# Kernel tuning notes

Hardware: AMD Instinct MI355X
Metric: run time of the kernel (lower is better)

Reference implementation:

```python
import jax, jax.numpy as jnp
import numpy as np

N_NODES = 100000
N_EDGES = 800000
F_IN, HID, N_CLS = 256, 128, 32


def setup_inputs() -> dict:
    key = jax.random.key(0)
    k1, k2, k3, k4, k5 = jax.random.split(key, 5)
    features = jax.random.normal(k1, (N_NODES, F_IN), dtype=jnp.float32)
    # random directed edges with no self loops (so add_remaining_self_loops == append all loops)
    src = jax.random.randint(k2, (N_EDGES,), 0, N_NODES)
    off = jax.random.randint(k3, (N_EDGES,), 1, N_NODES)
    dst = (src + off) % N_NODES
    edge_index = jnp.stack([src, dst]).astype(jnp.int64)
    # Glorot-style params for the two GCNConv layers
    W1 = jax.random.normal(k4, (F_IN, HID), dtype=jnp.float32) * (1.0 / np.sqrt(F_IN))
    b1 = jnp.zeros((HID,), dtype=jnp.float32)
    W2 = jax.random.normal(k5, (HID, N_CLS), dtype=jnp.float32) * (1.0 / np.sqrt(HID))
    b2 = jnp.zeros((N_CLS,), dtype=jnp.float32)
    return {"features": features, "edge_index": edge_index, "W1": W1, "b1": b1, "W2": W2, "b2": b2}


def _gcn_conv(x, W, b, src, dst, norm, n):
    xw = x @ W                                  # [N, d_out] dense GEMM
    msg = xw[src] * norm[:, None]               # gather + scale, [E, d_out]
    out = jax.ops.segment_sum(msg, dst, num_segments=n)  # scatter-add to targets
    return out + b


def reference(features, edge_index, W1, b1, W2, b2):
    n = features.shape[0]
    # add_remaining_self_loops (input has none, so append all)
    loops = jnp.arange(n, dtype=edge_index.dtype)
    src = jnp.concatenate([edge_index[0], loops])
    dst = jnp.concatenate([edge_index[1], loops])
    # gcn_norm: deg over targets, sym normalization deg^-1/2 A deg^-1/2
    deg = jax.ops.segment_sum(jnp.ones_like(src, dtype=features.dtype), dst, num_segments=n)
    dinv = jnp.where(deg > 0, jax.lax.rsqrt(deg), 0.0)
    norm = dinv[src] * dinv[dst]
    x = _gcn_conv(features, W1, b1, src, dst, norm, n)
    x = jax.nn.relu(x)
    # dropout is identity at inference (training=False)
    x = _gcn_conv(x, W2, b2, src, dst, norm, n)
    return jax.nn.log_softmax(x, axis=1)
```

## Files before the change

### kernel.cpp

```cpp
#include <hip/hip_runtime.h>
#include <hip/hip_bf16.h>

typedef __bf16 bf16_t;
typedef __attribute__((ext_vector_type(8))) __bf16 bf16x8;
typedef __attribute__((ext_vector_type(4))) float f32x4;

__device__ inline void packB_one(const float* __restrict__ B, bf16_t* __restrict__ Bp,
                                 int N, int idx) {
    int j    = idx & 7;
    int lane = (idx >> 3) & 63;
    int st   = idx >> 9;
    int nt   = N >> 4;
    int s = st / nt, t = st - s * nt;
    int k = s * 32 + (lane >> 4) * 8 + j;
    int n = t * 16 + (lane & 15);
    Bp[idx] = (bf16_t)B[(size_t)k * N + n];
}

__global__ __launch_bounds__(256) void k_front(
        const float* __restrict__ W1, bf16_t* __restrict__ Bp1,
        const float* __restrict__ W2, bf16_t* __restrict__ Bp2,
        const int* __restrict__ dst, int* __restrict__ deg, int E) {
    int b = blockIdx.x, t = threadIdx.x;
    const int PACK_BLOCKS = (32768 + 4096) / 256;
    if (b < PACK_BLOCKS) {
        int idx = b * 256 + t;
        if (idx < 32768) packB_one(W1, Bp1, 128, idx);
        else             packB_one(W2, Bp2, 32, idx - 32768);
        return;
    }
    int i = (b - PACK_BLOCKS) * 1024 + t * 4;
    if (i + 4 <= E) {
        int4 v = *(const int4*)(dst + i);
        atomicAdd(&deg[v.x], 1); atomicAdd(&deg[v.y], 1);
        atomicAdd(&deg[v.z], 1); atomicAdd(&deg[v.w], 1);
    } else {
#pragma unroll
        for (int j = 0; j < 4; ++j)
            if (i + j < E) atomicAdd(&deg[dst[i + j]], 1);
    }
}

__global__ __launch_bounds__(256) void k_dinv_scan1(const int* __restrict__ deg,
                                                    float* __restrict__ dinv,
                                                    int* __restrict__ bsum, int n) {
    __shared__ int red[256];
    int b = blockIdx.x, t = threadIdx.x;
    int base = b * 1024 + t * 4;
    int s = 0;
#pragma unroll
    for (int j = 0; j < 4; ++j) {
        int i = base + j;
        if (i < n) { int d = deg[i]; s += d; dinv[i] = rsqrtf((float)(d + 1)); }
    }
    red[t] = s;
    __syncthreads();
    for (int d = 128; d > 0; d >>= 1) {
        if (t < d) red[t] += red[t + d];
        __syncthreads();
    }
    if (t == 0) bsum[b] = red[0];
}

__global__ __launch_bounds__(256) void k_scan2(int* __restrict__ bsum, int nb,
                                               int* __restrict__ rowPtr, int n) {
    __shared__ int s[256];
    int t = threadIdx.x;
    int v = (t < nb) ? bsum[t] : 0;
    s[t] = v;
    __syncthreads();
    for (int d = 1; d < 256; d <<= 1) {
        int u = (t >= d) ? s[t - d] : 0;
        __syncthreads();
        s[t] += u;
        __syncthreads();
    }
    if (t < nb) bsum[t] = s[t] - v;
    if (t == 255) rowPtr[n] = s[255];
}

__global__ __launch_bounds__(256) void k_scan3(const int* __restrict__ deg,
                                               const int* __restrict__ bsum,
                                               int* __restrict__ rowPtr,
                                               int* __restrict__ cursor, int n) {
    __shared__ int red[256];
    int b = blockIdx.x, t = threadIdx.x;
    int base = b * 1024 + t * 4;
    int v[4]; int s = 0;
#pragma unroll
    for (int j = 0; j < 4; ++j) { int i = base + j; v[j] = (i < n) ? deg[i] : 0; s += v[j]; }
    red[t] = s;
    __syncthreads();
    for (int d = 1; d < 256; d <<= 1) {
        int u = (t >= d) ? red[t - d] : 0;
        __syncthreads();
        red[t] += u;
        __syncthreads();
    }
    int run = bsum[b] + red[t] - s;
#pragma unroll
    for (int j = 0; j < 4; ++j) {
        int i = base + j;
        if (i < n) { rowPtr[i] = run; cursor[i] = run; run += v[j]; }
    }
}

template <int KSTEPS, int NTILES>
__global__ __launch_bounds__(256) void k_gemm_scatter(
        const float* __restrict__ A, const bf16_t* __restrict__ Bp,
        bf16_t* __restrict__ C, int M, int gemmBlocks,
        const int* __restrict__ src, const int* __restrict__ dst,
        const float* __restrict__ dinv, int* __restrict__ cursor,
        int2* __restrict__ edata, int E) {
    int b = blockIdx.x, t = threadIdx.x;
    if (b < gemmBlocks) {
        int wave = (b * 256 + t) >> 6;
        if (wave * 16 >= M) return;
        int lane = t & 63;
        int r16 = lane & 15, quad = lane >> 4;
        const int K = KSTEPS * 32, N = NTILES * 16;
        f32x4 acc[NTILES] = {};
        const float* arow = A + (size_t)(wave * 16 + r16) * K + quad * 8;
#pragma unroll
        for (int s = 0; s < KSTEPS; ++s) {
            const float* ap = arow + s * 32;
            bf16x8 a;
#pragma unroll
            for (int j = 0; j < 8; ++j) a[j] = (bf16_t)ap[j];
            const bf16_t* bp = Bp + ((size_t)(s * NTILES) * 64 + lane) * 8;
#pragma unroll
            for (int tt = 0; tt < NTILES; ++tt) {
                bf16x8 bb = *(const bf16x8*)(bp + tt * 512);
                acc[tt] = __builtin_amdgcn_mfma_f32_16x16x32_bf16(a, bb, acc[tt], 0, 0, 0);
            }
        }
#pragma unroll
        for (int tt = 0; tt < NTILES; ++tt)
#pragma unroll
            for (int r = 0; r < 4; ++r)
                C[(size_t)(wave * 16 + quad * 4 + r) * N + tt * 16 + r16] = (bf16_t)acc[tt][r];
        return;
    }
    int e = (b - gemmBlocks) * 256 + t;
    if (e >= E) return;
    int s = src[e], d = dst[e];
    int pos = atomicAdd(&cursor[d], 1);
    int2 p; p.x = s; p.y = __float_as_int(dinv[s] * dinv[d]);
    edata[pos] = p;
}

template <int KSTEPS, int NTILES>
__global__ __launch_bounds__(256) void k_gemm_pa16(
        const bf16_t* __restrict__ A, const bf16_t* __restrict__ Bp,
        bf16_t* __restrict__ C, int M) {
    int wave = (blockIdx.x * blockDim.x + threadIdx.x) >> 6;
    if (wave * 16 >= M) return;
    int lane = threadIdx.x & 63;
    int r16 = lane & 15, quad = lane >> 4;
    const int K = KSTEPS * 32, N = NTILES * 16;
    f32x4 acc[NTILES] = {};
    const bf16_t* arow = A + (size_t)(wave * 16 + r16) * K + quad * 8;
#pragma unroll
    for (int s = 0; s < KSTEPS; ++s) {
        bf16x8 a = *(const bf16x8*)(arow + s * 32);
        const bf16_t* bp = Bp + ((size_t)(s * NTILES) * 64 + lane) * 8;
#pragma unroll
        for (int t = 0; t < NTILES; ++t) {
            bf16x8 b = *(const bf16x8*)(bp + t * 512);
            acc[t] = __builtin_amdgcn_mfma_f32_16x16x32_bf16(a, b, acc[t], 0, 0, 0);
        }
    }
#pragma unroll
    for (int t = 0; t < NTILES; ++t)
#pragma unroll
        for (int r = 0; r < 4; ++r)
            C[(size_t)(wave * 16 + quad * 4 + r) * N + t * 16 + r16] = (bf16_t)acc[t][r];
}

__global__ __launch_bounds__(256) void k_agg1(
        const int* __restrict__ rowPtr, const int2* __restrict__ edata,
        const bf16_t* __restrict__ XW1, const float* __restrict__ dinv,
        const float* __restrict__ b1, bf16_t* __restrict__ H, int n) {
    int wave = (blockIdx.x * blockDim.x + threadIdx.x) >> 6;
    if (wave >= n) return;
    int lane = threadIdx.x & 63;
    int fl = (lane & 15) << 3;
    int h  = lane >> 4;
    int r0 = rowPtr[wave], r1 = rowPtr[wave + 1];
    float a0[8] = {}, a1[8] = {};
    int k = r0 + h;
    for (; k + 4 < r1; k += 8) {
        int2 e0 = edata[k], e1 = edata[k + 4];
        float w0 = __int_as_float(e0.y), w1 = __int_as_float(e1.y);
        bf16x8 x0 = *(const bf16x8*)(XW1 + ((size_t)e0.x << 7) + fl);
        bf16x8 x1 = *(const bf16x8*)(XW1 + ((size_t)e1.x << 7) + fl);
#pragma unroll
        for (int j = 0; j < 8; ++j) { a0[j] += (float)x0[j] * w0; a1[j] += (float)x1[j] * w1; }
    }
    if (k < r1) {
        int2 e0 = edata[k];
        float w0 = __int_as_float(e0.y);
        bf16x8 x0 = *(const bf16x8*)(XW1 + ((size_t)e0.x << 7) + fl);
#pragma unroll
        for (int j = 0; j < 8; ++j) a0[j] += (float)x0[j] * w0;
    }
#pragma unroll
    for (int j = 0; j < 8; ++j) {
        a0[j] += a1[j];
        a0[j] += __shfl_xor(a0[j], 16);
        a0[j] += __shfl_xor(a0[j], 32);
    }
    if (h == 0) {
        float d = dinv[wave], d2 = d * d;
        bf16x8 xs = *(const bf16x8*)(XW1 + ((size_t)wave << 7) + fl);
        bf16x8 hv;
#pragma unroll
        for (int j = 0; j < 8; ++j) {
            float v = a0[j] + (float)xs[j] * d2 + b1[fl + j];
            hv[j] = (bf16_t)fmaxf(v, 0.f);
        }
        *(bf16x8*)(H + ((size_t)wave << 7) + fl) = hv;
    }
}

__global__ __launch_bounds__(256) void k_agg2(
        const int* __restrict__ rowPtr, const int2* __restrict__ edata,
        const bf16_t* __restrict__ XW2, const float* __restrict__ dinv,
        const float* __restrict__ b2, float* __restrict__ out, int n) {
    int wave = (blockIdx.x * blockDim.x + threadIdx.x) >> 6;
    if (wave >= n) return;
    int lane = threadIdx.x & 63;
    int g = lane & 15;
    int h = lane >> 4;
    int r0 = rowPtr[wave], r1 = rowPtr[wave + 1];
    float a00 = 0.f, a01 = 0.f, a10 = 0.f, a11 = 0.f;
    int k = r0 + h;
    for (; k + 4 < r1; k += 8) {
        int2 e0 = edata[k], e1 = edata[k + 4];
        float w0 = __int_as_float(e0.y), w1 = __int_as_float(e1.y);
        unsigned p0 = *(const unsigned*)(XW2 + ((size_t)e0.x << 5) + 2 * g);
        unsigned p1 = *(const unsigned*)(XW2 + ((size_t)e1.x << 5) + 2 * g);
        a00 += __int_as_float(p0 << 16) * w0;
        a01 += __int_as_float(p0 & 0xffff0000u) * w0;
        a10 += __int_as_float(p1 << 16) * w1;
        a11 += __int_as_float(p1 & 0xffff0000u) * w1;
    }
    if (k < r1) {
        int2 e0 = edata[k];
        float w0 = __int_as_float(e0.y);
        unsigned p0 = *(const unsigned*)(XW2 + ((size_t)e0.x << 5) + 2 * g);
        a00 += __int_as_float(p0 << 16) * w0;
        a01 += __int_as_float(p0 & 0xffff0000u) * w0;
    }
    float v0 = a00 + a10, v1 = a01 + a11;
    v0 += __shfl_xor(v0, 16); v0 += __shfl_xor(v0, 32);
    v1 += __shfl_xor(v1, 16); v1 += __shfl_xor(v1, 32);
    float d = dinv[wave], d2 = d * d;
    unsigned ps = *(const unsigned*)(XW2 + ((size_t)wave << 5) + 2 * g);
    float2 bb = *(const float2*)(b2 + 2 * g);
    v0 += __int_as_float(ps << 16) * d2 + bb.x;
    v1 += __int_as_float(ps & 0xffff0000u) * d2 + bb.y;
    float mx = fmaxf(v0, v1);
#pragma unroll
    for (int m = 8; m >= 1; m >>= 1) mx = fmaxf(mx, __shfl_xor(mx, m));
    float s = expf(v0 - mx) + expf(v1 - mx);
#pragma unroll
    for (int m = 8; m >= 1; m >>= 1) s += __shfl_xor(s, m);
    if (h == 0) {
        float ls = logf(s);
        float2 o; o.x = v0 - mx - ls; o.y = v1 - mx - ls;
        *(float2*)(out + ((size_t)wave << 5) + 2 * g) = o;
    }
}

extern "C" void kernel_launch(void* const* d_in, const int* in_sizes, int n_in,
                              void* d_out, int out_size, void* d_ws, size_t ws_size,
                              hipStream_t stream) {
    const float* feat = (const float*)d_in[0];
    const int*   eidx = (const int*)d_in[1];
    const float* W1   = (const float*)d_in[2];
    const float* b1   = (const float*)d_in[3];
    const float* W2   = (const float*)d_in[4];
    const float* b2   = (const float*)d_in[5];
    float* out = (float*)d_out;

    const int FIN = 256, HID = 128, NCLS = 32;
    const int N = in_sizes[0] / FIN;
    const int E = in_sizes[1] / 2;
    const int* src = eidx;
    const int* dst = eidx + E;

    char* ws = (char*)d_ws;
    size_t o = 0;
    auto alloc = [&](size_t bytes) -> void* {
        void* p = ws + o;
        o = (o + bytes + 255) & ~(size_t)255;
        return p;
    };
    int*    deg    = (int*)   alloc((size_t)N * 4);
    int*    cursor = (int*)   alloc((size_t)N * 4);
    float*  dinv   = (float*) alloc((size_t)N * 4);
    int*    rowPtr = (int*)   alloc((size_t)(N + 1) * 4);
    int*    bsum   = (int*)   alloc(256 * 4);
    bf16_t* Bp1    = (bf16_t*)alloc((size_t)(FIN / 32) * (HID / 16) * 512 * 2);
    bf16_t* Bp2    = (bf16_t*)alloc((size_t)(HID / 32) * (NCLS / 16) * 512 * 2);
    int2*   edata  = (int2*)  alloc((size_t)E * 8);
    bf16_t* XW1    = (bf16_t*)alloc((size_t)N * HID * 2);
    bf16_t* H      = (bf16_t*)alloc((size_t)N * HID * 2);
    bf16_t* XW2    = XW1;

    const int T = 256;
    const int NB = (N + 1023) >> 10;
    const int PACK_BLOCKS = (32768 + 4096) / 256;
    const int DEG_BLOCKS  = (E + 1023) / 1024;
    hipMemsetAsync(deg, 0, (size_t)N * 4, stream);
    k_front     <<<PACK_BLOCKS + DEG_BLOCKS, T, 0, stream>>>(W1, Bp1, W2, Bp2, dst, deg, E);
    k_dinv_scan1<<<NB, T, 0, stream>>>(deg, dinv, bsum, N);
    k_scan2     <<<1, T, 0, stream>>>(bsum, NB, rowPtr, N);
    k_scan3     <<<NB, T, 0, stream>>>(deg, bsum, rowPtr, cursor, N);

    {
        int waves = (N + 15) / 16;
        int gemmBlocks = (waves * 64 + T - 1) / T;
        int scatBlocks = (E + T - 1) / T;
        k_gemm_scatter<8, 8><<<gemmBlocks + scatBlocks, T, 0, stream>>>(
            feat, Bp1, XW1, N, gemmBlocks, src, dst, dinv, cursor, edata, E);
    }
    k_agg1<<<(N * 64 + T - 1) / T, T, 0, stream>>>(rowPtr, edata, XW1, dinv, b1, H, N);

    {
        int waves = (N + 15) / 16;
        k_gemm_pa16<4, 2><<<(waves * 64 + T - 1) / T, T, 0, stream>>>(H, Bp2, XW2, N);
    }
    k_agg2<<<(N * 64 + T - 1) / T, T, 0, stream>>>(rowPtr, edata, XW2, dinv, b2, out, N);
}
```

Baseline: 343.3 us.

## Pre-pack features and hidden activations into MFMA fragment layout for GEMMs

Adds a pass in the front kernel that converts the fp32 features into bf16 stored in the MFMA A-fragment order, so the first GEMM does one 16-byte load per K-step instead of eight strided fp32 loads and conversions. The layer-1 aggregation now writes H directly in that packed fragment order, so the second GEMM reads it contiguously. The cost is an extra full read of the features plus a write of a new bf16 buffer before the GEMM, which adds HBM traffic. The packed H stores are also more scattered.

```diff
diff --git a/kernel.cpp b/kernel.cpp
--- a/kernel.cpp
+++ b/kernel.cpp
@@ -18,10 +18,31 @@
 }
 
 __global__ __launch_bounds__(256) void k_front(
+        const float* __restrict__ feat, bf16_t* __restrict__ Ap,
         const float* __restrict__ W1, bf16_t* __restrict__ Bp1,
         const float* __restrict__ W2, bf16_t* __restrict__ Bp2,
-        const int* __restrict__ dst, int* __restrict__ deg, int E) {
+        const int* __restrict__ dst, int* __restrict__ deg,
+        int N_nodes, int E, int APACK_BLOCKS) {
     int b = blockIdx.x, t = threadIdx.x;
+    if (b < APACK_BLOCKS) {
+        int idx = b * 256 + t;
+        if (idx >= N_nodes * 64) return;
+        int w    = idx >> 6;
+        int lane = idx & 63;
+        int r16 = lane & 15, quad = lane >> 4;
+        const float* arow = feat + (size_t)(w * 16 + r16) * 256 + quad * 8;
+        bf16_t* opb = Ap + (size_t)w * 4096 + lane * 8;
+#pragma unroll
+        for (int s = 0; s < 8; ++s) {
+            const float* ap = arow + s * 32;
+            bf16x8 a;
+#pragma unroll
+            for (int j = 0; j < 8; ++j) a[j] = (bf16_t)ap[j];
+            *(bf16x8*)(opb + s * 512) = a;
+        }
+        return;
+    }
+    b -= APACK_BLOCKS;
     const int PACK_BLOCKS = (32768 + 4096) / 256;
     if (b < PACK_BLOCKS) {
         int idx = b * 256 + t;
@@ -107,7 +128,7 @@
 
 template <int KSTEPS, int NTILES>
 __global__ __launch_bounds__(256) void k_gemm_scatter(
-        const float* __restrict__ A, const bf16_t* __restrict__ Bp,
+        const bf16_t* __restrict__ Ap, const bf16_t* __restrict__ Bp,
         bf16_t* __restrict__ C, int M, int gemmBlocks,
         const int* __restrict__ src, const int* __restrict__ dst,
         const float* __restrict__ dinv, int* __restrict__ cursor,
@@ -118,15 +139,12 @@
         if (wave * 16 >= M) return;
         int lane = t & 63;
         int r16 = lane & 15, quad = lane >> 4;
-        const int K = KSTEPS * 32, N = NTILES * 16;
+        const int N = NTILES * 16;
         f32x4 acc[NTILES] = {};
-        const float* arow = A + (size_t)(wave * 16 + r16) * K + quad * 8;
+        const bf16_t* apb = Ap + (size_t)wave * (KSTEPS * 512) + lane * 8;
 #pragma unroll
         for (int s = 0; s < KSTEPS; ++s) {
-            const float* ap = arow + s * 32;
-            bf16x8 a;
-#pragma unroll
-            for (int j = 0; j < 8; ++j) a[j] = (bf16_t)ap[j];
+            bf16x8 a = *(const bf16x8*)(apb + s * 512);
             const bf16_t* bp = Bp + ((size_t)(s * NTILES) * 64 + lane) * 8;
 #pragma unroll
             for (int tt = 0; tt < NTILES; ++tt) {
@@ -150,19 +168,19 @@
 }
 
 template <int KSTEPS, int NTILES>
-__global__ __launch_bounds__(256) void k_gemm_pa16(
-        const bf16_t* __restrict__ A, const bf16_t* __restrict__ Bp,
+__global__ __launch_bounds__(256) void k_gemm_p(
+        const bf16_t* __restrict__ Ap, const bf16_t* __restrict__ Bp,
         bf16_t* __restrict__ C, int M) {
     int wave = (blockIdx.x * blockDim.x + threadIdx.x) >> 6;
     if (wave * 16 >= M) return;
     int lane = threadIdx.x & 63;
     int r16 = lane & 15, quad = lane >> 4;
-    const int K = KSTEPS * 32, N = NTILES * 16;
+    const int N = NTILES * 16;
     f32x4 acc[NTILES] = {};
-    const bf16_t* arow = A + (size_t)(wave * 16 + r16) * K + quad * 8;
+    const bf16_t* apb = Ap + (size_t)wave * (KSTEPS * 512) + lane * 8;
 #pragma unroll
     for (int s = 0; s < KSTEPS; ++s) {
-        bf16x8 a = *(const bf16x8*)(arow + s * 32);
+        bf16x8 a = *(const bf16x8*)(apb + s * 512);
         const bf16_t* bp = Bp + ((size_t)(s * NTILES) * 64 + lane) * 8;
 #pragma unroll
         for (int t = 0; t < NTILES; ++t) {
@@ -180,7 +198,7 @@
 __global__ __launch_bounds__(256) void k_agg1(
         const int* __restrict__ rowPtr, const int2* __restrict__ edata,
         const bf16_t* __restrict__ XW1, const float* __restrict__ dinv,
-        const float* __restrict__ b1, bf16_t* __restrict__ H, int n) {
+        const float* __restrict__ b1, bf16_t* __restrict__ Hp, int n) {
     int wave = (blockIdx.x * blockDim.x + threadIdx.x) >> 6;
     if (wave >= n) return;
     int lane = threadIdx.x & 63;
@@ -219,7 +237,10 @@
             float v = a0[j] + (float)xs[j] * d2 + b1[fl + j];
             hv[j] = (bf16_t)fmaxf(v, 0.f);
         }
-        *(bf16x8*)(H + ((size_t)wave << 7) + fl) = hv;
+        int q = lane & 15;
+        size_t off = (((size_t)(wave >> 4) * 4 + (q >> 2)) * 64
+                      + (wave & 15) + 16 * (q & 3)) * 8;
+        *(bf16x8*)(Hp + off) = hv;
     }
 }
 
@@ -305,16 +326,20 @@
     bf16_t* Bp1    = (bf16_t*)alloc((size_t)(FIN / 32) * (HID / 16) * 512 * 2);
     bf16_t* Bp2    = (bf16_t*)alloc((size_t)(HID / 32) * (NCLS / 16) * 512 * 2);
     int2*   edata  = (int2*)  alloc((size_t)E * 8);
+    bf16_t* Ap1    = (bf16_t*)alloc((size_t)N * FIN * 2);
     bf16_t* XW1    = (bf16_t*)alloc((size_t)N * HID * 2);
-    bf16_t* H      = (bf16_t*)alloc((size_t)N * HID * 2);
+    bf16_t* Hp     = (bf16_t*)alloc((size_t)N * HID * 2);
     bf16_t* XW2    = XW1;
 
     const int T = 256;
     const int NB = (N + 1023) >> 10;
+    const int APACK_BLOCKS = (N * 64 + T - 1) / T;
+    const int AB = ((N / 16) * 64 + T - 1) / T;
     const int PACK_BLOCKS = (32768 + 4096) / 256;
     const int DEG_BLOCKS  = (E + 1023) / 1024;
     hipMemsetAsync(deg, 0, (size_t)N * 4, stream);
-    k_front     <<<PACK_BLOCKS + DEG_BLOCKS, T, 0, stream>>>(W1, Bp1, W2, Bp2, dst, deg, E);
+    k_front     <<<AB + PACK_BLOCKS + DEG_BLOCKS, T, 0, stream>>>(
+        feat, Ap1, W1, Bp1, W2, Bp2, dst, deg, N / 16 * 16 * 4 , E, AB);
     k_dinv_scan1<<<NB, T, 0, stream>>>(deg, dinv, bsum, N);
     k_scan2     <<<1, T, 0, stream>>>(bsum, NB, rowPtr, N);
     k_scan3     <<<NB, T, 0, stream>>>(deg, bsum, rowPtr, cursor, N);
@@ -324,13 +349,13 @@
         int gemmBlocks = (waves * 64 + T - 1) / T;
         int scatBlocks = (E + T - 1) / T;
         k_gemm_scatter<8, 8><<<gemmBlocks + scatBlocks, T, 0, stream>>>(
-            feat, Bp1, XW1, N, gemmBlocks, src, dst, dinv, cursor, edata, E);
-    }
-    k_agg1<<<(N * 64 + T - 1) / T, T, 0, stream>>>(rowPtr, edata, XW1, dinv, b1, H, N);
+            Ap1, Bp1, XW1, N, gemmBlocks, src, dst, dinv, cursor, edata, E);
+    }
+    k_agg1<<<(N * 64 + T - 1) / T, T, 0, stream>>>(rowPtr, edata, XW1, dinv, b1, Hp, N);
 
     {
         int waves = (N + 15) / 16;
-        k_gemm_pa16<4, 2><<<(waves * 64 + T - 1) / T, T, 0, stream>>>(H, Bp2, XW2, N);
+        k_gemm_p<4, 2><<<(waves * 64 + T - 1) / T, T, 0, stream>>>(Hp, Bp2, XW2, N);
     }
     k_agg2<<<(N * 64 + T - 1) / T, T, 0, stream>>>(rowPtr, edata, XW2, dinv, b2, out, N);
 }
```

Result: slower. 353.7 us (+3.0%).
